# Performance work log

Measured on AMD Instinct MI355X. Metric: run time of the kernel, lower is better.

Reference implementation:

```python
import jax, jax.numpy as jnp
import numpy as np

IN_FEATURES = 1_000_000
OUT_FEATURE_SETS = 4
NUM_CHUNKS = 2500
SPLIT_SIZE = 400  # ceil(IN_FEATURES / NUM_CHUNKS); padding = 0 here
BATCH = 64


def setup_inputs() -> dict:
    key = jax.random.key(0)
    k1, k2, k3 = jax.random.split(key, 3)
    x = jax.random.normal(k1, (BATCH, IN_FEATURES), dtype=jnp.float32)
    weight = jax.random.normal(k2, (OUT_FEATURE_SETS, SPLIT_SIZE, NUM_CHUNKS), dtype=jnp.float32)
    bias = jax.random.normal(k3, (OUT_FEATURE_SETS * NUM_CHUNKS,), dtype=jnp.float32)
    return {"x": x, "weight": weight, "bias": bias}


def reference(x, weight, bias):
    # weight: [O, S, C]
    O, S, C = weight.shape
    B = x.shape[0]
    pad = S * C - x.shape[1]
    if pad > 0:
        x = jnp.pad(x, ((0, 0), (0, pad)))
    xr = x.reshape(B, S, C)  # [B, S, C]
    # per set o: sum over split dim S, keep chunk dim C -> [B, O, C]
    out = jnp.einsum('bsc,osc->boc', xr, weight)
    # torch cat over sets along dim=1 => set-major flatten [B, O*C]
    return out.reshape(B, O * C) + bias
```

## Files before the change

### kernel.cpp

```cpp
#include <hip/hip_runtime.h>


constexpr int IN_F   = 1000000;
constexpr int S_DIM  = 400;
constexpr int C_DIM  = 2500;
constexpr int O_SETS = 4;
constexpr int B_SZ   = 64;
constexpr int OC     = O_SETS * C_DIM;
constexpr int OUT_N  = B_SZ * OC;

constexpr int NQ      = C_DIM / 4;
constexpr int THREADS = 640;
constexpr int NSPLIT  = 8;
constexpr int SSEG    = S_DIM / NSPLIT;
constexpr int BT      = 2;
constexpr int BGRP    = B_SZ / BT;
constexpr int STEPQ   = NQ;

typedef float f4 __attribute__((ext_vector_type(4)));

__device__ __forceinline__ f4 ntload(const f4* p) {
    return __builtin_nontemporal_load(p);
}

__device__ __forceinline__ void fma4(f4& a, f4 p, f4 q) {
    a.x = fmaf(p.x, q.x, a.x);
    a.y = fmaf(p.y, q.y, a.y);
    a.z = fmaf(p.z, q.z, a.z);
    a.w = fmaf(p.w, q.w, a.w);
}

__global__ __launch_bounds__(256) void sl_bias_init(const float* __restrict__ bias,
                                                    float* __restrict__ out) {
    const int t = blockIdx.x * 256 + threadIdx.x;
    if (t >= OUT_N / 4) return;
    const int idx = t * 4;
    const int oc  = idx % OC;
    *(f4*)(out + idx) = *(const f4*)(bias + oc);
}

__global__ __launch_bounds__(THREADS, 3) void sl_part_atomic(const float* __restrict__ x,
                                                             const float* __restrict__ w,
                                                             float* __restrict__ out) {
    const int tid = threadIdx.x;
    const bool act = (tid < NQ);
    const int q   = act ? tid : NQ - 1;
    const int z   = blockIdx.x;
    const int b0  = blockIdx.y * BT;
    const int s0  = z * SSEG;

    const f4* xp[BT];
#pragma unroll
    for (int i = 0; i < BT; ++i)
        xp[i] = (const f4*)(x + (size_t)(b0 + i) * IN_F + (size_t)s0 * C_DIM) + q;

    const f4* wp[O_SETS];
#pragma unroll
    for (int o = 0; o < O_SETS; ++o)
        wp[o] = (const f4*)(w + (size_t)o * (S_DIM * C_DIM) + (size_t)s0 * C_DIM) + q;

    f4 acc[BT][O_SETS];
#pragma unroll
    for (int i = 0; i < BT; ++i)
#pragma unroll
        for (int o = 0; o < O_SETS; ++o)
            acc[i][o] = (f4)(0.f);

    f4 xb[3][BT], wb[3][O_SETS];
#pragma unroll
    for (int p = 0; p < 2; ++p) {
#pragma unroll
        for (int i = 0; i < BT; ++i) { xb[p][i] = ntload(xp[i]); xp[i] += STEPQ; }
#pragma unroll
        for (int o = 0; o < O_SETS; ++o) { wb[p][o] = *wp[o]; wp[o] += STEPQ; }
    }

#pragma unroll
    for (int s = 0; s < SSEG; ++s) {
        const int cur = s % 3;
        const int nxt = (s + 2) % 3;
        if (s + 2 < SSEG) {
#pragma unroll
            for (int i = 0; i < BT; ++i) { xb[nxt][i] = ntload(xp[i]); xp[i] += STEPQ; }
#pragma unroll
            for (int o = 0; o < O_SETS; ++o) { wb[nxt][o] = *wp[o]; wp[o] += STEPQ; }
        }
#pragma unroll
        for (int i = 0; i < BT; ++i)
#pragma unroll
            for (int o = 0; o < O_SETS; ++o)
                fma4(acc[i][o], xb[cur][i], wb[cur][o]);
    }

    if (act) {
#pragma unroll
        for (int i = 0; i < BT; ++i) {
            float* orow = out + (size_t)(b0 + i) * OC;
#pragma unroll
            for (int o = 0; o < O_SETS; ++o) {
                float* dst = orow + o * C_DIM + q * 4;
                atomicAdd(dst + 0, acc[i][o].x);
                atomicAdd(dst + 1, acc[i][o].y);
                atomicAdd(dst + 2, acc[i][o].z);
                atomicAdd(dst + 3, acc[i][o].w);
            }
        }
    }
}

extern "C" void kernel_launch(void* const* d_in, const int* in_sizes, int n_in,
                              void* d_out, int out_size, void* d_ws, size_t ws_size,
                              hipStream_t stream) {
    const float* x    = (const float*)d_in[0];
    const float* wgt  = (const float*)d_in[1];
    const float* bias = (const float*)d_in[2];
    float* out = (float*)d_out;

    sl_bias_init<<<(OUT_N / 4 + 255) / 256, 256, 0, stream>>>(bias, out);
    dim3 g(NSPLIT, BGRP);
    sl_part_atomic<<<g, THREADS, 0, stream>>>(x, wgt, out);
}
```

Before: 418.6 us.

## Fuse bias and full S reduction per thread, removing atomics and split-S

Replaces the split-S kernel that used atomic adds with a single kernel. Each thread reduces all 400 split rows for one batch row and one 4-wide chunk slice, then adds bias and stores directly. This removes the bias-init launch and the atomic traffic, and uses deeper register prefetch queues for x and w. In exchange the grid has fewer, partially idle blocks, and the weights are re-read once per batch row, which may reduce memory-level parallelism.

New measurement: 401.4 us. 1.04x faster.

```diff
diff --git a/kernel.cpp b/kernel.cpp
--- a/kernel.cpp
+++ b/kernel.cpp
@@ -10,12 +10,12 @@
 constexpr int OUT_N  = B_SZ * OC;
 
 constexpr int NQ      = C_DIM / 4;
-constexpr int THREADS = 640;
-constexpr int NSPLIT  = 8;
-constexpr int SSEG    = S_DIM / NSPLIT;
-constexpr int BT      = 2;
-constexpr int BGRP    = B_SZ / BT;
+constexpr int NCHUNK  = 8;
+constexpr int CHUNK   = 80;
+constexpr int THREADS = 128;
 constexpr int STEPQ   = NQ;
+constexpr int XD      = 8;
+constexpr int WD      = 4;
 
 typedef float f4 __attribute__((ext_vector_type(4)));
 
@@ -30,81 +30,68 @@
     a.w = fmaf(p.w, q.w, a.w);
 }
 
-__global__ __launch_bounds__(256) void sl_bias_init(const float* __restrict__ bias,
-                                                    float* __restrict__ out) {
-    const int t = blockIdx.x * 256 + threadIdx.x;
-    if (t >= OUT_N / 4) return;
-    const int idx = t * 4;
-    const int oc  = idx % OC;
-    *(f4*)(out + idx) = *(const f4*)(bias + oc);
-}
+__global__ __launch_bounds__(THREADS, 2) void sl_fused(const float* __restrict__ x,
+                                                       const float* __restrict__ w,
+                                                       const float* __restrict__ bias,
+                                                       float* __restrict__ out) {
+    const int tid = threadIdx.x;
+    const int cb  = blockIdx.x;
+    const int b   = blockIdx.y;
+    const int q   = cb * CHUNK + tid;
+    if (tid >= CHUNK || q >= NQ) return;
 
-__global__ __launch_bounds__(THREADS, 3) void sl_part_atomic(const float* __restrict__ x,
-                                                             const float* __restrict__ w,
-                                                             float* __restrict__ out) {
-    const int tid = threadIdx.x;
-    const bool act = (tid < NQ);
-    const int q   = act ? tid : NQ - 1;
-    const int z   = blockIdx.x;
-    const int b0  = blockIdx.y * BT;
-    const int s0  = z * SSEG;
-
-    const f4* xp[BT];
-#pragma unroll
-    for (int i = 0; i < BT; ++i)
-        xp[i] = (const f4*)(x + (size_t)(b0 + i) * IN_F + (size_t)s0 * C_DIM) + q;
-
+    const f4* xp = (const f4*)(x + (size_t)b * IN_F) + q;
     const f4* wp[O_SETS];
 #pragma unroll
     for (int o = 0; o < O_SETS; ++o)
-        wp[o] = (const f4*)(w + (size_t)o * (S_DIM * C_DIM) + (size_t)s0 * C_DIM) + q;
+        wp[o] = (const f4*)(w + (size_t)o * (S_DIM * C_DIM)) + q;
 
-    f4 acc[BT][O_SETS];
+    f4 acc[O_SETS];
 #pragma unroll
-    for (int i = 0; i < BT; ++i)
+    for (int o = 0; o < O_SETS; ++o) acc[o] = (f4)(0.f);
+
+    f4 xb[XD];
+    f4 wb[WD][O_SETS];
 #pragma unroll
-        for (int o = 0; o < O_SETS; ++o)
-            acc[i][o] = (f4)(0.f);
-
-    f4 xb[3][BT], wb[3][O_SETS];
+    for (int p = 0; p < XD; ++p) { xb[p] = ntload(xp); xp += STEPQ; }
 #pragma unroll
-    for (int p = 0; p < 2; ++p) {
-#pragma unroll
-        for (int i = 0; i < BT; ++i) { xb[p][i] = ntload(xp[i]); xp[i] += STEPQ; }
+    for (int p = 0; p < WD; ++p)
 #pragma unroll
         for (int o = 0; o < O_SETS; ++o) { wb[p][o] = *wp[o]; wp[o] += STEPQ; }
+
+    for (int sb = 0; sb < S_DIM - 8; sb += 8) {
+#pragma unroll
+        for (int u = 0; u < 8; ++u) {
+#pragma unroll
+            for (int o = 0; o < O_SETS; ++o) fma4(acc[o], xb[u], wb[u % WD][o]);
+            xb[u] = ntload(xp); xp += STEPQ;
+#pragma unroll
+            for (int o = 0; o < O_SETS; ++o) { wb[u % WD][o] = *wp[o]; wp[o] += STEPQ; }
+        }
+    }
+#pragma unroll
+    for (int u = 0; u < 4; ++u) {
+#pragma unroll
+        for (int o = 0; o < O_SETS; ++o) fma4(acc[o], xb[u], wb[u][o]);
+#pragma unroll
+        for (int o = 0; o < O_SETS; ++o) { wb[u][o] = *wp[o]; wp[o] += STEPQ; }
+    }
+#pragma unroll
+    for (int u = 4; u < 8; ++u) {
+#pragma unroll
+        for (int o = 0; o < O_SETS; ++o) fma4(acc[o], xb[u], wb[u - 4][o]);
     }
 
+    float* orow = out + (size_t)b * OC;
 #pragma unroll
-    for (int s = 0; s < SSEG; ++s) {
-        const int cur = s % 3;
-        const int nxt = (s + 2) % 3;
-        if (s + 2 < SSEG) {
-#pragma unroll
-            for (int i = 0; i < BT; ++i) { xb[nxt][i] = ntload(xp[i]); xp[i] += STEPQ; }
-#pragma unroll
-            for (int o = 0; o < O_SETS; ++o) { wb[nxt][o] = *wp[o]; wp[o] += STEPQ; }
-        }
-#pragma unroll
-        for (int i = 0; i < BT; ++i)
-#pragma unroll
-            for (int o = 0; o < O_SETS; ++o)
-                fma4(acc[i][o], xb[cur][i], wb[cur][o]);
-    }
-
-    if (act) {
-#pragma unroll
-        for (int i = 0; i < BT; ++i) {
-            float* orow = out + (size_t)(b0 + i) * OC;
-#pragma unroll
-            for (int o = 0; o < O_SETS; ++o) {
-                float* dst = orow + o * C_DIM + q * 4;
-                atomicAdd(dst + 0, acc[i][o].x);
-                atomicAdd(dst + 1, acc[i][o].y);
-                atomicAdd(dst + 2, acc[i][o].z);
-                atomicAdd(dst + 3, acc[i][o].w);
-            }
-        }
+    for (int o = 0; o < O_SETS; ++o) {
+        f4 bv = *(const f4*)(bias + o * C_DIM + q * 4);
+        f4 r;
+        r.x = acc[o].x + bv.x;
+        r.y = acc[o].y + bv.y;
+        r.z = acc[o].z + bv.z;
+        r.w = acc[o].w + bv.w;
+        __builtin_nontemporal_store(r, (f4*)(orow + o * C_DIM + q * 4));
     }
 }
 
@@ -116,7 +103,6 @@
     const float* bias = (const float*)d_in[2];
     float* out = (float*)d_out;
 
-    sl_bias_init<<<(OUT_N / 4 + 255) / 256, 256, 0, stream>>>(bias, out);
-    dim3 g(NSPLIT, BGRP);
-    sl_part_atomic<<<g, THREADS, 0, stream>>>(x, wgt, out);
+    dim3 g(NCHUNK, B_SZ);
+    sl_fused<<<g, THREADS, 0, stream>>>(x, wgt, bias, out);
 }
```
